# Performance work log

Hardware: AMD Instinct MI355X
Metric: run time of the kernel (lower is better)

The kernel has to match this reference:

```python
import jax, jax.numpy as jnp
import numpy as np

B, S, H, E = 64, 512, 1024, 10  # batch, encoder seq len, hidden, n_events
LSTM_IN = H + 1 + E  # context (H) + x (1) + sim_scores (E)


def setup_inputs() -> dict:
    key = jax.random.key(0)
    ks = jax.random.split(key, 20)
    s = 0.02
    return {
        "x": jax.random.normal(ks[0], (B, 1), jnp.float32),
        "h0": jax.random.normal(ks[1], (1, B, H), jnp.float32),
        "c0": jax.random.normal(ks[2], (1, B, H), jnp.float32),
        "encoder_output": jax.random.normal(ks[3], (B, S, H), jnp.float32),
        "W_enc": jax.random.normal(ks[4], (H, H), jnp.float32) * s,
        "W_dec": jax.random.normal(ks[5], (H, H), jnp.float32) * s,
        "w_val": jax.random.normal(ks[6], (H,), jnp.float32) * s,
        "W_gate": jax.random.normal(ks[7], (E, E), jnp.float32) * s,
        "events_mat": jax.random.normal(ks[8], (E, H), jnp.float32) * s,
        "W_ih": jax.random.normal(ks[9], (4 * H, LSTM_IN), jnp.float32) * s,
        "W_hh": jax.random.normal(ks[10], (4 * H, H), jnp.float32) * s,
        "b_ih": jax.random.normal(ks[11], (4 * H,), jnp.float32) * s,
        "b_hh": jax.random.normal(ks[12], (4 * H,), jnp.float32) * s,
        "ln_g": jnp.ones((H,), jnp.float32),
        "ln_b": jnp.zeros((H,), jnp.float32),
        "W_fin": jax.random.normal(ks[13], (1, H), jnp.float32) * s,
        "b_fin": jnp.zeros((1,), jnp.float32),
    }


def reference(x, h0, c0, encoder_output, W_enc, W_dec, w_val, W_gate,
              events_mat, W_ih, W_hh, b_ih, b_hh, ln_g, ln_b, W_fin, b_fin):
    h = h0[0]  # [B,H] (num_layers == 1)
    c = c0[0]
    # Bahdanau attention: v^T tanh(W_e enc + W_d h)
    proj = jnp.einsum('bsh,gh->bsg', encoder_output, W_enc) + (h @ W_dec.T)[:, None, :]
    attn_scores = jnp.tanh(proj) @ w_val  # [B,S]
    attn_weight = jax.nn.softmax(attn_scores, axis=1)
    context = jnp.einsum('bs,bsh->bh', attn_weight, encoder_output)  # [B,H]
    # event similarity + gate
    sim_scores = (context @ events_mat.T) @ W_gate.T  # [B,E]
    # single-step LSTM on concat(context, sim, x)
    xin = jnp.concatenate([context, sim_scores, x], axis=1)  # [B, H+E+1]
    gates = xin @ W_ih.T + b_ih + h @ W_hh.T + b_hh  # [B,4H]
    i, f, g, o = jnp.split(gates, 4, axis=1)  # torch gate order: i,f,g,o
    c_new = jax.nn.sigmoid(f) * c + jax.nn.sigmoid(i) * jnp.tanh(g)
    h_new = jax.nn.sigmoid(o) * jnp.tanh(c_new)  # [B,H]
    # LayerNorm(eps=1e-5)
    mu = jnp.mean(h_new, axis=-1, keepdims=True)
    var = jnp.mean(jnp.square(h_new - mu), axis=-1, keepdims=True)
    y = (h_new - mu) / jnp.sqrt(var + 1e-5) * ln_g + ln_b
    fin_output = y @ W_fin.T + b_fin  # [B,1]
    return fin_output, (h_new[None], c_new[None]), attn_weight, sim_scores
```

## Files before the change

### kernel.cpp

```cpp
#include <hip/hip_runtime.h>
#include <math.h>

#define Bn 64
#define Sn 512
#define Hn 1024
#define En 10
#define Mn (Bn*Sn)
#define KIN 1035
#define KP  2112

#define OUT_FIN 0
#define OUT_H   64
#define OUT_C   65600
#define OUT_AW  131136
#define OUT_SIM 163904

#define WS_ENCB  0
#define WS_WENCB 16777216
#define WS_DECP  17301504
#define WS_PART  17367040
#define WS_CTX   17629184
#define WS_XINT  17694720
#define WS_WCATB 0
#define WS_GPART 4325376
#define WS_XINB  6422528

typedef __attribute__((ext_vector_type(8))) short bf16x8;
typedef __attribute__((ext_vector_type(4))) float f32x4;

#define ASYNC_CP16(gptr, lptr) \
  __builtin_amdgcn_global_load_lds((const __attribute__((address_space(1))) void*)(gptr), \
                                   (__attribute__((address_space(3))) void*)(lptr), 16, 0, 0)

static __device__ __forceinline__ unsigned short f2bf(float f) {
    union { float f; unsigned int u; } v; v.f = f;
    unsigned int r = (v.u + 0x7fffu + ((v.u >> 16) & 1u)) >> 16;
    return (unsigned short)r;
}
static __device__ __forceinline__ float bf2f(unsigned short h) {
    union { unsigned int u; float f; } v; v.u = ((unsigned int)h) << 16;
    return v.f;
}

__global__ __launch_bounds__(256) void k_cast(const float* __restrict__ enc,
                                              const float* __restrict__ Wenc,
                                              unsigned short* __restrict__ encB,
                                              unsigned short* __restrict__ wencB) {
    const float* src; unsigned short* dst; size_t off;
    if (blockIdx.x < 16384) {
        src = enc; dst = encB;
        off = ((size_t)blockIdx.x * 256 + threadIdx.x) * 8;
    } else {
        src = Wenc; dst = wencB;
        off = ((size_t)(blockIdx.x - 16384) * 256 + threadIdx.x) * 8;
    }
    float4 v0 = *(const float4*)(src + off);
    float4 v1 = *(const float4*)(src + off + 4);
    ushort4 a; a.x = f2bf(v0.x); a.y = f2bf(v0.y); a.z = f2bf(v0.z); a.w = f2bf(v0.w);
    ushort4 b; b.x = f2bf(v1.x); b.y = f2bf(v1.y); b.z = f2bf(v1.z); b.w = f2bf(v1.w);
    *(ushort4*)(dst + off)     = a;
    *(ushort4*)(dst + off + 4) = b;
}

__global__ __launch_bounds__(256) void k0_h0T(const float* __restrict__ h0,
                                              float* __restrict__ xinT) {
    int idx = blockIdx.x * 256 + threadIdx.x;
    int b = idx >> 10;
    int h = idx & 1023;
    xinT[(1035 + h) * 64 + b] = h0[idx];
}

__global__ __launch_bounds__(256) void k1_decproj(const float* __restrict__ xinT,
                                                  const float* __restrict__ Wdec,
                                                  float* __restrict__ decp) {
    int g = blockIdx.x * 4 + (threadIdx.x >> 6);
    int b = threadIdx.x & 63;
    const float* w = Wdec + (size_t)g * 1024;
    float a0 = 0.f, a1 = 0.f, a2 = 0.f, a3 = 0.f;
    for (int k = 0; k < 1024; k += 4) {
        a0 += xinT[(1035 + k + 0) * 64 + b] * w[k + 0];
        a1 += xinT[(1035 + k + 1) * 64 + b] * w[k + 1];
        a2 += xinT[(1035 + k + 2) * 64 + b] * w[k + 2];
        a3 += xinT[(1035 + k + 3) * 64 + b] * w[k + 3];
    }
    decp[b * 1024 + g] = (a0 + a1) + (a2 + a3);
}

__global__ __launch_bounds__(256) void k2_scores(const unsigned short* __restrict__ encB,
                                                 const unsigned short* __restrict__ wencB,
                                                 const float* __restrict__ decp,
                                                 const float* __restrict__ wval,
                                                 float* __restrict__ part) {
    __shared__ short As[8192];
    __shared__ short Bs[8192];
    __shared__ float rsum[2][128];

    const int m0 = blockIdx.x * 128;
    const int n0 = blockIdx.y * 128;
    const int b  = m0 >> 9;
    const int tid  = threadIdx.x;
    const int wave = tid >> 6;
    const int lane = tid & 63;
    const int wr = wave >> 1;
    const int wc = wave & 1;
    const int q4 = lane >> 4;
    const int ml = lane & 15;

    f32x4 acc[4][4];
#pragma unroll
    for (int i = 0; i < 4; ++i)
#pragma unroll
        for (int j = 0; j < 4; ++j) acc[i][j] = (f32x4){0.f, 0.f, 0.f, 0.f};

    const unsigned short* aTile = encB  + (size_t)m0 * 1024;
    const unsigned short* bTile = wencB + (size_t)n0 * 1024;

    for (int k0 = 0; k0 < 1024; k0 += 64) {
        __syncthreads();
#pragma unroll
        for (int t = 0; t < 4; ++t) {
            int cc = t * 4 + wave;
            int q  = cc >> 1;
            int mb = (cc & 1) << 6;
            ASYNC_CP16(aTile + (size_t)(mb + lane) * 1024 + k0 + q * 8,
                       &As[(q * 128 + mb) * 8]);
            ASYNC_CP16(bTile + (size_t)(mb + lane) * 1024 + k0 + q * 8,
                       &Bs[(q * 128 + mb) * 8]);
        }
        __syncthreads();
#pragma unroll
        for (int s = 0; s < 2; ++s) {
            bf16x8 af[4], bfr[4];
#pragma unroll
            for (int i = 0; i < 4; ++i)
                af[i] = *(const bf16x8*)&As[((((s << 2) + q4) * 128) + wr * 64 + (i << 4) + ml) * 8];
#pragma unroll
            for (int j = 0; j < 4; ++j)
                bfr[j] = *(const bf16x8*)&Bs[((((s << 2) + q4) * 128) + wc * 64 + (j << 4) + ml) * 8];
#pragma unroll
            for (int i = 0; i < 4; ++i)
#pragma unroll
                for (int j = 0; j < 4; ++j)
                    acc[i][j] = __builtin_amdgcn_mfma_f32_16x16x32_bf16(af[i], bfr[j], acc[i][j], 0, 0, 0);
        }
    }

    float dpv[4], wvv[4];
#pragma unroll
    for (int j = 0; j < 4; ++j) {
        int n = n0 + wc * 64 + (j << 4) + ml;
        dpv[j] = decp[b * 1024 + n];
        wvv[j] = wval[n];
    }
#pragma unroll
    for (int i = 0; i < 4; ++i) {
#pragma unroll
        for (int r = 0; r < 4; ++r) {
            float p = 0.f;
#pragma unroll
            for (int j = 0; j < 4; ++j) p += tanhf(acc[i][j][r] + dpv[j]) * wvv[j];
            p += __shfl_xor(p, 1);
            p += __shfl_xor(p, 2);
            p += __shfl_xor(p, 4);
            p += __shfl_xor(p, 8);
            if (ml == 0) rsum[wc][wr * 64 + (i << 4) + q4 * 4 + r] = p;
        }
    }
    __syncthreads();
    if (tid < 128)
        part[(size_t)blockIdx.y * Mn + m0 + tid] = rsum[0][tid] + rsum[1][tid];
}

__device__ __forceinline__ float block_sum256(float v, float* red, int tid) {
#pragma unroll
    for (int off = 1; off < 64; off <<= 1) v += __shfl_xor(v, off);
    if ((tid & 63) == 0) red[tid >> 6] = v;
    __syncthreads();
    v = red[0] + red[1] + red[2] + red[3];
    __syncthreads();
    return v;
}

__global__ __launch_bounds__(256) void k3a_softmax(const float* __restrict__ part,
                                                   float* __restrict__ wts,
                                                   float* __restrict__ out) {
    int b = blockIdx.x;
    int tid = threadIdx.x;
    __shared__ float red[8];
    int s0 = tid, s1 = tid + 256;
    float v0 = 0.f, v1 = 0.f;
#pragma unroll
    for (int nb = 0; nb < 8; ++nb) {
        v0 += part[(size_t)nb * Mn + b * 512 + s0];
        v1 += part[(size_t)nb * Mn + b * 512 + s1];
    }
    float mx = fmaxf(v0, v1);
#pragma unroll
    for (int off = 1; off < 64; off <<= 1) mx = fmaxf(mx, __shfl_xor(mx, off));
    if ((tid & 63) == 0) red[tid >> 6] = mx;
    __syncthreads();
    mx = fmaxf(fmaxf(red[0], red[1]), fmaxf(red[2], red[3]));
    __syncthreads();
    float e0 = __expf(v0 - mx), e1 = __expf(v1 - mx);
    float sm = block_sum256(e0 + e1, red, tid);
    float inv = 1.0f / sm;
    float w0 = e0 * inv, w1 = e1 * inv;
    wts[b * 512 + s0] = w0;
    wts[b * 512 + s1] = w1;
    out[OUT_AW + b * 512 + s0] = w0;
    out[OUT_AW + b * 512 + s1] = w1;
}

__global__ __launch_bounds__(256) void k3b_context(const unsigned short* __restrict__ encB,
                                                   const float* __restrict__ wts,
                                                   float* __restrict__ ctx) {
    int b = blockIdx.y;
    int h2 = (blockIdx.x * 256 + threadIdx.x) * 2;
    const unsigned short* e = encB + (size_t)b * Sn * Hn + h2;
    const float* w = wts + b * 512;
    float a0 = 0.f, a1 = 0.f, b0 = 0.f, b1 = 0.f;
    for (int s = 0; s < 512; s += 2) {
        unsigned int p0 = *(const unsigned int*)(e + (size_t)(s + 0) * 1024);
        unsigned int p1 = *(const unsigned int*)(e + (size_t)(s + 1) * 1024);
        a0 += w[s + 0] * bf2f((unsigned short)(p0 & 0xffffu));
        b0 += w[s + 0] * bf2f((unsigned short)(p0 >> 16));
        a1 += w[s + 1] * bf2f((unsigned short)(p1 & 0xffffu));
        b1 += w[s + 1] * bf2f((unsigned short)(p1 >> 16));
    }
    ctx[b * 1024 + h2]     = a0 + a1;
    ctx[b * 1024 + h2 + 1] = b0 + b1;
}

__global__ __launch_bounds__(256) void k4_sim(const float* __restrict__ ctx,
                                              const float* __restrict__ events,
                                              const float* __restrict__ Wg,
                                              float* __restrict__ out) {
    int b = blockIdx.x;
    int tid = threadIdx.x, wv = tid >> 6, lane = tid & 63;
    __shared__ float tmp[16];
    const float* c = ctx + b * 1024;
    for (int e = wv; e < 10; e += 4) {
        const float* ev = events + e * 1024;
        float a = 0.f;
#pragma unroll
        for (int kk = 0; kk < 1024; kk += 64) a += c[kk + lane] * ev[kk + lane];
#pragma unroll
        for (int off = 1; off < 64; off <<= 1) a += __shfl_xor(a, off);
        if (lane == 0) tmp[e] = a;
    }
    __syncthreads();
    if (tid < 10) {
        float s2 = 0.f;
#pragma unroll
        for (int e = 0; e < 10; ++e) s2 += Wg[tid * 10 + e] * tmp[e];
        out[OUT_SIM + b * 10 + tid] = s2;
    }
}

__global__ __launch_bounds__(256) void k_castW(const float* __restrict__ Wih,
                                               const float* __restrict__ Whh,
                                               unsigned short* __restrict__ WcatB) {
    unsigned int idx = blockIdx.x * 256 + threadIdx.x;
    unsigned int r = idx / KP;
    unsigned int k = idx - r * KP;
    float v = 0.f;
    if (k < 1035)      v = Wih[(size_t)r * 1035 + k];
    else if (k < 2059) v = Whh[(size_t)r * 1024 + (k - 1035)];
    WcatB[idx] = f2bf(v);
}

__global__ __launch_bounds__(256) void k_xinB(const float* __restrict__ ctx,
                                              const float* __restrict__ simOut,
                                              const float* __restrict__ x,
                                              const float* __restrict__ h0,
                                              unsigned short* __restrict__ xinB) {
    unsigned int idx = blockIdx.x * 256 + threadIdx.x;
    unsigned int b = idx / KP;
    unsigned int k = idx - b * KP;
    float v = 0.f;
    if (k < 1024)       v = ctx[b * 1024 + k];
    else if (k < 1034)  v = simOut[b * 10 + (k - 1024)];
    else if (k == 1034) v = x[b];
    else if (k < 2059)  v = h0[b * 1024 + (k - 1035)];
    xinB[idx] = f2bf(v);
}

__global__ __launch_bounds__(256) void k5_gemm(const unsigned short* __restrict__ xinB,
                                               const unsigned short* __restrict__ WcatB,
                                               float* __restrict__ gpart) {
    __shared__ short As[4096];
    __shared__ short Bs[8192];

    const int n0 = blockIdx.x * 128;
    const int sp = blockIdx.y;
    const int kbeg   = (sp == 0) ? 0 : (5 + (sp - 1) * 4) * 64;
    const int ksteps = (sp == 0) ? 5 : 4;
    const int tid  = threadIdx.x;
    const int wave = tid >> 6;
    const int lane = tid & 63;
    const int wr = wave >> 1;
    const int wc = wave & 1;
    const int q4 = lane >> 4;
    const int ml = lane & 15;

    f32x4 acc[2][4];
#pragma unroll
    for (int i = 0; i < 2; ++i)
#pragma unroll
        for (int j = 0; j < 4; ++j) acc[i][j] = (f32x4){0.f, 0.f, 0.f, 0.f};

    const unsigned short* bTile = WcatB + (size_t)n0 * KP;

    for (int kk = 0; kk < ksteps; ++kk) {
        int k0 = kbeg + kk * 64;
        __syncthreads();
#pragma unroll
        for (int t = 0; t < 2; ++t) {
            int q = wave * 2 + t;
            ASYNC_CP16(xinB + (size_t)lane * KP + k0 + q * 8, &As[(q * 64) * 8]);
        }
#pragma unroll
        for (int t = 0; t < 4; ++t) {
            int cb = t * 4 + wave;
            int q  = cb >> 1;
            int mb = (cb & 1) << 6;
            ASYNC_CP16(bTile + (size_t)(mb + lane) * KP + k0 + q * 8,
                       &Bs[(q * 128 + mb) * 8]);
        }
        __syncthreads();
#pragma unroll
        for (int s = 0; s < 2; ++s) {
            bf16x8 af[2], bfr[4];
#pragma unroll
            for (int i = 0; i < 2; ++i)
                af[i] = *(const bf16x8*)&As[((((s << 2) + q4) * 64) + wr * 32 + (i << 4) + ml) * 8];
#pragma unroll
            for (int j = 0; j < 4; ++j)
                bfr[j] = *(const bf16x8*)&Bs[((((s << 2) + q4) * 128) + wc * 64 + (j << 4) + ml) * 8];
#pragma unroll
            for (int i = 0; i < 2; ++i)
#pragma unroll
                for (int j = 0; j < 4; ++j)
                    acc[i][j] = __builtin_amdgcn_mfma_f32_16x16x32_bf16(af[i], bfr[j], acc[i][j], 0, 0, 0);
        }
    }

#pragma unroll
    for (int i = 0; i < 2; ++i)
#pragma unroll
        for (int j = 0; j < 4; ++j)
#pragma unroll
            for (int r = 0; r < 4; ++r) {
                int m = wr * 32 + (i << 4) + q4 * 4 + r;
                int n = n0 + wc * 64 + (j << 4) + ml;
                gpart[((size_t)sp * 64 + m) * 4096 + n] = acc[i][j][r];
            }
}

__global__ __launch_bounds__(256) void k5_fin(const float* __restrict__ gpart,
                                              const float* __restrict__ bih,
                                              const float* __restrict__ bhh,
                                              const float* __restrict__ c0,
                                              float* __restrict__ out) {
    int idx = blockIdx.x * 256 + threadIdx.x;
    int b = idx >> 10;
    int u = idx & 1023;
    float g[4];
#pragma unroll
    for (int gt = 0; gt < 4; ++gt) {
        int r = gt * 1024 + u;
        float a = bih[r] + bhh[r];
#pragma unroll
        for (int sp = 0; sp < 8; ++sp)
            a += gpart[((size_t)sp * 64 + b) * 4096 + r];
        g[gt] = a;
    }
    float cp = c0[b * 1024 + u];
    float si = 1.f / (1.f + __expf(-g[0]));
    float sf = 1.f / (1.f + __expf(-g[1]));
    float so = 1.f / (1.f + __expf(-g[3]));
    float cn = sf * cp + si * tanhf(g[2]);
    float hn = so * tanhf(cn);
    out[OUT_H + b * 1024 + u] = hn;
    out[OUT_C + b * 1024 + u] = cn;
}

__global__ __launch_bounds__(256) void k6_lnfin(const float* __restrict__ lng,
                                                const float* __restrict__ lnb,
                                                const float* __restrict__ Wfin,
                                                const float* __restrict__ bfin,
                                                float* __restrict__ out) {
    int b = blockIdx.x, tid = threadIdx.x;
    __shared__ float red[8];
    const float* h = out + OUT_H + b * 1024;
    float v0 = h[tid], v1 = h[tid + 256], v2 = h[tid + 512], v3 = h[tid + 768];
    float mu = block_sum256(v0 + v1 + v2 + v3, red, tid) * (1.f / 1024.f);
    float d0 = v0 - mu, d1 = v1 - mu, d2 = v2 - mu, d3 = v3 - mu;
    float var = block_sum256(d0 * d0 + d1 * d1 + d2 * d2 + d3 * d3, red, tid) * (1.f / 1024.f);
    float rstd = rsqrtf(var + 1e-5f);
    float acc = (d0 * rstd * lng[tid]       + lnb[tid])       * Wfin[tid]
              + (d1 * rstd * lng[tid + 256] + lnb[tid + 256]) * Wfin[tid + 256]
              + (d2 * rstd * lng[tid + 512] + lnb[tid + 512]) * Wfin[tid + 512]
              + (d3 * rstd * lng[tid + 768] + lnb[tid + 768]) * Wfin[tid + 768];
    acc = block_sum256(acc, red, tid);
    if (tid == 0) out[OUT_FIN + b] = acc + bfin[0];
}

extern "C" void kernel_launch(void* const* d_in, const int* in_sizes, int n_in,
                              void* d_out, int out_size, void* d_ws, size_t ws_size,
                              hipStream_t stream) {
    (void)in_sizes; (void)n_in; (void)out_size; (void)ws_size;
    const float* x    = (const float*)d_in[0];
    const float* h0   = (const float*)d_in[1];
    const float* c0   = (const float*)d_in[2];
    const float* enc  = (const float*)d_in[3];
    const float* Wenc = (const float*)d_in[4];
    const float* Wdec = (const float*)d_in[5];
    const float* wval = (const float*)d_in[6];
    const float* Wg   = (const float*)d_in[7];
    const float* ev   = (const float*)d_in[8];
    const float* Wih  = (const float*)d_in[9];
    const float* Whh  = (const float*)d_in[10];
    const float* bih  = (const float*)d_in[11];
    const float* bhh  = (const float*)d_in[12];
    const float* lng  = (const float*)d_in[13];
    const float* lnb  = (const float*)d_in[14];
    const float* Wfin = (const float*)d_in[15];
    const float* bfin = (const float*)d_in[16];

    float* out  = (float*)d_out;
    float* ws   = (float*)d_ws;
    unsigned short* encB  = (unsigned short*)(ws + WS_ENCB);
    unsigned short* wencB = (unsigned short*)(ws + WS_WENCB);
    float* decp = ws + WS_DECP;
    float* part = ws + WS_PART;
    float* ctx  = ws + WS_CTX;
    float* xinT = ws + WS_XINT;
    float* wts  = ws + WS_DECP;
    unsigned short* WcatB = (unsigned short*)(ws + WS_WCATB);
    float* gpart = ws + WS_GPART;
    unsigned short* xinB  = (unsigned short*)(ws + WS_XINB);

    k_cast     <<<16896, 256, 0, stream>>>(enc, Wenc, encB, wencB);
    k0_h0T     <<<256, 256, 0, stream>>>(h0, xinT);
    k1_decproj <<<256, 256, 0, stream>>>(xinT, Wdec, decp);
    k2_scores  <<<dim3(256, 8), 256, 0, stream>>>(encB, wencB, decp, wval, part);
    k3a_softmax<<<64, 256, 0, stream>>>(part, wts, out);
    k3b_context<<<dim3(2, 64), 256, 0, stream>>>(encB, wts, ctx);
    k4_sim     <<<64, 256, 0, stream>>>(ctx, ev, Wg, out);
    k_castW    <<<33792, 256, 0, stream>>>(Wih, Whh, WcatB);
    k_xinB     <<<528, 256, 0, stream>>>(ctx, out + OUT_SIM, x, h0, xinB);
    k5_gemm    <<<dim3(32, 8), 256, 0, stream>>>(xinB, WcatB, gpart);
    k5_fin     <<<256, 256, 0, stream>>>(gpart, bih, bhh, c0, out);
    k6_lnfin   <<<64, 256, 0, stream>>>(lng, lnb, Wfin, bfin, out);
}
```

Before: 523.7 us.

## Use MFMA for decoder projection, split context over S, widen score tiles

The decoder-hidden projection now casts W_dec and h0 to bf16 inside the existing cast kernel and computes it with a split-K MFMA GEMM, removing the transpose and scalar matvec kernels. The score GEMM uses 512-thread blocks with a 128-wide K step and a fast exp-based tanh. The context reduction is split into four S-chunks per batch to launch more blocks, followed by a small reduction kernel. In exchange, the decoder projection now uses bf16 inputs, tanh is approximated, and there are extra partial buffers and one more launch.

```diff
diff --git a/kernel.cpp b/kernel.cpp
--- a/kernel.cpp
+++ b/kernel.cpp
@@ -17,10 +17,12 @@
 
 #define WS_ENCB  0
 #define WS_WENCB 16777216
-#define WS_DECP  17301504
-#define WS_PART  17367040
-#define WS_CTX   17629184
-#define WS_XINT  17694720
+#define WS_WTS   17301504
+#define WS_PART  17334272
+#define WS_CTX   17596416
+#define WS_WDECB 17661952
+#define WS_H0B   18186240
+#define WS_DPART 18219008
 #define WS_WCATB 0
 #define WS_GPART 4325376
 #define WS_XINB  6422528
@@ -41,19 +43,27 @@
     union { unsigned int u; float f; } v; v.u = ((unsigned int)h) << 16;
     return v.f;
 }
+static __device__ __forceinline__ float fast_tanh(float x) {
+    float cx = fminf(15.f, fmaxf(-15.f, x));
+    float e = __expf(2.f * cx);
+    return (e - 1.f) * __builtin_amdgcn_rcpf(e + 1.f);
+}
 
 __global__ __launch_bounds__(256) void k_cast(const float* __restrict__ enc,
                                               const float* __restrict__ Wenc,
+                                              const float* __restrict__ Wdec,
+                                              const float* __restrict__ h0,
                                               unsigned short* __restrict__ encB,
-                                              unsigned short* __restrict__ wencB) {
+                                              unsigned short* __restrict__ wencB,
+                                              unsigned short* __restrict__ wdecB,
+                                              unsigned short* __restrict__ h0B) {
+    int bid = blockIdx.x;
     const float* src; unsigned short* dst; size_t off;
-    if (blockIdx.x < 16384) {
-        src = enc; dst = encB;
-        off = ((size_t)blockIdx.x * 256 + threadIdx.x) * 8;
-    } else {
-        src = Wenc; dst = wencB;
-        off = ((size_t)(blockIdx.x - 16384) * 256 + threadIdx.x) * 8;
-    }
+    if (bid < 16384)      { src = enc;  dst = encB;  off = (size_t)bid * 2048; }
+    else if (bid < 16896) { src = Wenc; dst = wencB; off = (size_t)(bid - 16384) * 2048; }
+    else if (bid < 17408) { src = Wdec; dst = wdecB; off = (size_t)(bid - 16896) * 2048; }
+    else                  { src = h0;   dst = h0B;   off = (size_t)(bid - 17408) * 2048; }
+    off += (size_t)threadIdx.x * 8;
     float4 v0 = *(const float4*)(src + off);
     float4 v1 = *(const float4*)(src + off + 4);
     ushort4 a; a.x = f2bf(v0.x); a.y = f2bf(v0.y); a.z = f2bf(v0.z); a.w = f2bf(v0.w);
@@ -62,38 +72,83 @@
     *(ushort4*)(dst + off + 4) = b;
 }
 
-__global__ __launch_bounds__(256) void k0_h0T(const float* __restrict__ h0,
-                                              float* __restrict__ xinT) {
-    int idx = blockIdx.x * 256 + threadIdx.x;
-    int b = idx >> 10;
-    int h = idx & 1023;
-    xinT[(1035 + h) * 64 + b] = h0[idx];
-}
-
-__global__ __launch_bounds__(256) void k1_decproj(const float* __restrict__ xinT,
-                                                  const float* __restrict__ Wdec,
-                                                  float* __restrict__ decp) {
-    int g = blockIdx.x * 4 + (threadIdx.x >> 6);
-    int b = threadIdx.x & 63;
-    const float* w = Wdec + (size_t)g * 1024;
-    float a0 = 0.f, a1 = 0.f, a2 = 0.f, a3 = 0.f;
-    for (int k = 0; k < 1024; k += 4) {
-        a0 += xinT[(1035 + k + 0) * 64 + b] * w[k + 0];
-        a1 += xinT[(1035 + k + 1) * 64 + b] * w[k + 1];
-        a2 += xinT[(1035 + k + 2) * 64 + b] * w[k + 2];
-        a3 += xinT[(1035 + k + 3) * 64 + b] * w[k + 3];
-    }
-    decp[b * 1024 + g] = (a0 + a1) + (a2 + a3);
-}
-
-__global__ __launch_bounds__(256) void k2_scores(const unsigned short* __restrict__ encB,
-                                                 const unsigned short* __restrict__ wencB,
-                                                 const float* __restrict__ decp,
-                                                 const float* __restrict__ wval,
-                                                 float* __restrict__ part) {
-    __shared__ short As[8192];
+__global__ __launch_bounds__(256) void k1_gemm(const unsigned short* __restrict__ h0B,
+                                               const unsigned short* __restrict__ wdecB,
+                                               float* __restrict__ dpart) {
+    __shared__ short As[4096];
     __shared__ short Bs[8192];
-    __shared__ float rsum[2][128];
+
+    const int n0 = blockIdx.x * 128;
+    const int sp = blockIdx.y;
+    const int kbeg = sp * 256;
+    const int tid  = threadIdx.x;
+    const int wave = tid >> 6;
+    const int lane = tid & 63;
+    const int wr = wave >> 1;
+    const int wc = wave & 1;
+    const int q4 = lane >> 4;
+    const int ml = lane & 15;
+
+    f32x4 acc[2][4];
+#pragma unroll
+    for (int i = 0; i < 2; ++i)
+#pragma unroll
+        for (int j = 0; j < 4; ++j) acc[i][j] = (f32x4){0.f, 0.f, 0.f, 0.f};
+
+    const unsigned short* bTile = wdecB + (size_t)n0 * 1024;
+
+    for (int kk = 0; kk < 4; ++kk) {
+        int k0 = kbeg + kk * 64;
+        __syncthreads();
+#pragma unroll
+        for (int t = 0; t < 2; ++t) {
+            int q = wave * 2 + t;
+            ASYNC_CP16(h0B + (size_t)lane * 1024 + k0 + q * 8, &As[(q * 64) * 8]);
+        }
+#pragma unroll
+        for (int t = 0; t < 4; ++t) {
+            int cb = t * 4 + wave;
+            int q  = cb >> 1;
+            int mb = (cb & 1) << 6;
+            ASYNC_CP16(bTile + (size_t)(mb + lane) * 1024 + k0 + q * 8,
+                       &Bs[(q * 128 + mb) * 8]);
+        }
+        __syncthreads();
+#pragma unroll
+        for (int s = 0; s < 2; ++s) {
+            bf16x8 af[2], bfr[4];
+#pragma unroll
+            for (int i = 0; i < 2; ++i)
+                af[i] = *(const bf16x8*)&As[((((s << 2) + q4) * 64) + wr * 32 + (i << 4) + ml) * 8];
+#pragma unroll
+            for (int j = 0; j < 4; ++j)
+                bfr[j] = *(const bf16x8*)&Bs[((((s << 2) + q4) * 128) + wc * 64 + (j << 4) + ml) * 8];
+#pragma unroll
+            for (int i = 0; i < 2; ++i)
+#pragma unroll
+                for (int j = 0; j < 4; ++j)
+                    acc[i][j] = __builtin_amdgcn_mfma_f32_16x16x32_bf16(af[i], bfr[j], acc[i][j], 0, 0, 0);
+        }
+    }
+#pragma unroll
+    for (int i = 0; i < 2; ++i)
+#pragma unroll
+        for (int j = 0; j < 4; ++j)
+#pragma unroll
+            for (int r = 0; r < 4; ++r) {
+                int m = wr * 32 + (i << 4) + q4 * 4 + r;
+                int n = n0 + wc * 64 + (j << 4) + ml;
+                dpart[((size_t)sp * 64 + m) * 1024 + n] = acc[i][j][r];
+            }
+}
+
+__global__ __launch_bounds__(512, 4) void k2_scores(const unsigned short* __restrict__ encB,
+                                                    const unsigned short* __restrict__ wencB,
+                                                    const float* __restrict__ dpart,
+                                                    const float* __restrict__ wval,
+                                                    float* __restrict__ part) {
+    __shared__ short As[16384];
+    __shared__ short Bs[16384];
 
     const int m0 = blockIdx.x * 128;
     const int n0 = blockIdx.y * 128;
@@ -106,39 +161,46 @@
     const int q4 = lane >> 4;
     const int ml = lane & 15;
 
-    f32x4 acc[4][4];
-#pragma unroll
-    for (int i = 0; i < 4; ++i)
+    f32x4 acc[2][4];
+#pragma unroll
+    for (int i = 0; i < 2; ++i)
 #pragma unroll
         for (int j = 0; j < 4; ++j) acc[i][j] = (f32x4){0.f, 0.f, 0.f, 0.f};
 
     const unsigned short* aTile = encB  + (size_t)m0 * 1024;
     const unsigned short* bTile = wencB + (size_t)n0 * 1024;
 
-    for (int k0 = 0; k0 < 1024; k0 += 64) {
+    for (int k0 = 0; k0 < 1024; k0 += 128) {
         __syncthreads();
 #pragma unroll
-        for (int t = 0; t < 4; ++t) {
-            int cc = t * 4 + wave;
-            int q  = cc >> 1;
-            int mb = (cc & 1) << 6;
-            ASYNC_CP16(aTile + (size_t)(mb + lane) * 1024 + k0 + q * 8,
-                       &As[(q * 128 + mb) * 8]);
-            ASYNC_CP16(bTile + (size_t)(mb + lane) * 1024 + k0 + q * 8,
-                       &Bs[(q * 128 + mb) * 8]);
+        for (int t = 0; t < 8; ++t) {
+            int c = t * 8 + wave;
+            if (c < 32) {
+                int q  = c >> 1;
+                int mb = (c & 1) << 6;
+                ASYNC_CP16(aTile + (size_t)(mb + lane) * 1024 + k0 + q * 8,
+                           &As[(q * 128 + mb) * 8]);
+            } else {
+                int c2 = c - 32;
+                int q  = c2 >> 1;
+                int mb = (c2 & 1) << 6;
+                ASYNC_CP16(bTile + (size_t)(mb + lane) * 1024 + k0 + q * 8,
+                           &Bs[(q * 128 + mb) * 8]);
+            }
         }
         __syncthreads();
 #pragma unroll
-        for (int s = 0; s < 2; ++s) {
-            bf16x8 af[4], bfr[4];
-#pragma unroll
-            for (int i = 0; i < 4; ++i)
-                af[i] = *(const bf16x8*)&As[((((s << 2) + q4) * 128) + wr * 64 + (i << 4) + ml) * 8];
+        for (int s = 0; s < 4; ++s) {
+            bf16x8 af[2], bfr[4];
+            int q = (s << 2) + q4;
+#pragma unroll
+            for (int i = 0; i < 2; ++i)
+                af[i] = *(const bf16x8*)&As[((q * 128) + wr * 32 + (i << 4) + ml) * 8];
 #pragma unroll
             for (int j = 0; j < 4; ++j)
-                bfr[j] = *(const bf16x8*)&Bs[((((s << 2) + q4) * 128) + wc * 64 + (j << 4) + ml) * 8];
-#pragma unroll
-            for (int i = 0; i < 4; ++i)
+                bfr[j] = *(const bf16x8*)&Bs[((q * 128) + wc * 64 + (j << 4) + ml) * 8];
+#pragma unroll
+            for (int i = 0; i < 2; ++i)
 #pragma unroll
                 for (int j = 0; j < 4; ++j)
                     acc[i][j] = __builtin_amdgcn_mfma_f32_16x16x32_bf16(af[i], bfr[j], acc[i][j], 0, 0, 0);
@@ -149,26 +211,31 @@
 #pragma unroll
     for (int j = 0; j < 4; ++j) {
         int n = n0 + wc * 64 + (j << 4) + ml;
-        dpv[j] = decp[b * 1024 + n];
+        float d = 0.f;
+#pragma unroll
+        for (int sp = 0; sp < 4; ++sp) d += dpart[((size_t)sp * 64 + b) * 1024 + n];
+        dpv[j] = d;
         wvv[j] = wval[n];
     }
-#pragma unroll
-    for (int i = 0; i < 4; ++i) {
+    __syncthreads();
+    float* rsum = (float*)As;
+#pragma unroll
+    for (int i = 0; i < 2; ++i) {
 #pragma unroll
         for (int r = 0; r < 4; ++r) {
             float p = 0.f;
 #pragma unroll
-            for (int j = 0; j < 4; ++j) p += tanhf(acc[i][j][r] + dpv[j]) * wvv[j];
+            for (int j = 0; j < 4; ++j) p += fast_tanh(acc[i][j][r] + dpv[j]) * wvv[j];
             p += __shfl_xor(p, 1);
             p += __shfl_xor(p, 2);
             p += __shfl_xor(p, 4);
             p += __shfl_xor(p, 8);
-            if (ml == 0) rsum[wc][wr * 64 + (i << 4) + q4 * 4 + r] = p;
+            if (ml == 0) rsum[wc * 128 + wr * 32 + (i << 4) + q4 * 4 + r] = p;
         }
     }
     __syncthreads();
     if (tid < 128)
-        part[(size_t)blockIdx.y * Mn + m0 + tid] = rsum[0][tid] + rsum[1][tid];
+        part[(size_t)blockIdx.y * Mn + m0 + tid] = rsum[tid] + rsum[128 + tid];
 }
 
 __device__ __forceinline__ float block_sum256(float v, float* red, int tid) {
@@ -213,13 +280,15 @@
 
 __global__ __launch_bounds__(256) void k3b_context(const unsigned short* __restrict__ encB,
                                                    const float* __restrict__ wts,
-                                                   float* __restrict__ ctx) {
-    int b = blockIdx.y;
-    int h2 = (blockIdx.x * 256 + threadIdx.x) * 2;
-    const unsigned short* e = encB + (size_t)b * Sn * Hn + h2;
-    const float* w = wts + b * 512;
+                                                   float* __restrict__ ctxp) {
+    int b  = blockIdx.y;
+    int sc = blockIdx.x >> 1;
+    int hh = blockIdx.x & 1;
+    int h2 = (hh * 256 + threadIdx.x) * 2;
+    const unsigned short* e = encB + (size_t)b * Sn * Hn + (size_t)sc * 128 * Hn + h2;
+    const float* w = wts + b * 512 + sc * 128;
     float a0 = 0.f, a1 = 0.f, b0 = 0.f, b1 = 0.f;
-    for (int s = 0; s < 512; s += 2) {
+    for (int s = 0; s < 128; s += 2) {
         unsigned int p0 = *(const unsigned int*)(e + (size_t)(s + 0) * 1024);
         unsigned int p1 = *(const unsigned int*)(e + (size_t)(s + 1) * 1024);
         a0 += w[s + 0] * bf2f((unsigned short)(p0 & 0xffffu));
@@ -227,8 +296,14 @@
         a1 += w[s + 1] * bf2f((unsigned short)(p1 & 0xffffu));
         b1 += w[s + 1] * bf2f((unsigned short)(p1 >> 16));
     }
-    ctx[b * 1024 + h2]     = a0 + a1;
-    ctx[b * 1024 + h2 + 1] = b0 + b1;
+    ctxp[((size_t)sc * 64 + b) * 1024 + h2]     = a0 + a1;
+    ctxp[((size_t)sc * 64 + b) * 1024 + h2 + 1] = b0 + b1;
+}
+
+__global__ __launch_bounds__(256) void k3c_reduce(const float* __restrict__ ctxp,
+                                                  float* __restrict__ ctx) {
+    int idx = blockIdx.x * 256 + threadIdx.x;
+    ctx[idx] = ctxp[idx] + ctxp[65536 + idx] + ctxp[131072 + idx] + ctxp[196608 + idx];
 }
 
 __global__ __launch_bounds__(256) void k4_sim(const float* __restrict__ ctx,
@@ -344,7 +419,6 @@
                     acc[i][j] = __builtin_amdgcn_mfma_f32_16x16x32_bf16(af[i], bfr[j], acc[i][j], 0, 0, 0);
         }
     }
-
 #pragma unroll
     for (int i = 0; i < 2; ++i)
 #pragma unroll
@@ -432,21 +506,23 @@
     float* ws   = (float*)d_ws;
     unsigned short* encB  = (unsigned short*)(ws + WS_ENCB);
     unsigned short* wencB = (unsigned short*)(ws + WS_WENCB);
-    float* decp = ws + WS_DECP;
-    float* part = ws + WS_PART;
-    float* ctx  = ws + WS_CTX;
-    float* xinT = ws + WS_XINT;
-    float* wts  = ws + WS_DECP;
+    unsigned short* wdecB = (unsigned short*)(ws + WS_WDECB);
+    unsigned short* h0B   = (unsigned short*)(ws + WS_H0B);
+    float* dpart = ws + WS_DPART;
+    float* wts   = ws + WS_WTS;
+    float* part  = ws + WS_PART;
+    float* ctxp  = ws + WS_PART;
+    float* ctx   = ws + WS_CTX;
     unsigned short* WcatB = (unsigned short*)(ws + WS_WCATB);
     float* gpart = ws + WS_GPART;
     unsigned short* xinB  = (unsigned short*)(ws + WS_XINB);
 
-    k_cast     <<<16896, 256, 0, stream>>>(enc, Wenc, encB, wencB);
-    k0_h0T     <<<256, 256, 0, stream>>>(h0, xinT);
-    k1_decproj <<<256, 256, 0, stream>>>(xinT, Wdec, decp);
-    k2_scores  <<<dim3(256, 8), 256, 0, stream>>>(encB, wencB, decp, wval, part);
+    k_cast     <<<17440, 256, 0, stream>>>(enc, Wenc, Wdec, h0, encB, wencB, wdecB, h0B);
+    k1_gemm    <<<dim3(8, 4), 256, 0, stream>>>(h0B, wdecB, dpart);
+    k2_scores  <<<dim3(256, 8), 512, 0, stream>>>(encB, wencB, dpart, wval, part);
     k3a_softmax<<<64, 256, 0, stream>>>(part, wts, out);
-    k3b_context<<<dim3(2, 64), 256, 0, stream>>>(encB, wts, ctx);
+    k3b_context<<<dim3(8, 64), 256, 0, stream>>>(encB, wts, ctxp);
+    k3c_reduce <<<256, 256, 0, stream>>>(ctxp, ctx);
     k4_sim     <<<64, 256, 0, stream>>>(ctx, ev, Wg, out);
     k_castW    <<<33792, 256, 0, stream>>>(Wih, Whh, WcatB);
     k_xinB     <<<528, 256, 0, stream>>>(ctx, out + OUT_SIM, x, h0, xinB);
```

After: 466.6 us. -10.9%, faster.
